# Kernel optimization log

Measured on AMD Instinct MI355X. Metric: run time of the kernel, lower is better.

The kernel has to match this reference:

```python
import jax, jax.numpy as jnp
from jax import lax
import numpy as np

# Constants from CVLNet utils (get_meter_per_pixel() and SatMap_original_sidelength)
METER_PER_PIXEL = 0.2
SATMAP_ORIGINAL_SIDELENGTH = 512.0
SHIFT_RANGE = 32
EPS = 1e-12


def _l2_normalize_per_sample(x):
    # F.normalize(x.reshape(B, -1)) : L2-normalize each sample over all elements
    B = x.shape[0]
    norm = jnp.linalg.norm(x.reshape(B, -1), axis=1)
    norm = jnp.maximum(norm, EPS).reshape((B,) + (1,) * (x.ndim - 1))
    return x / norm


def setup_inputs() -> dict:
    key = jax.random.key(0)
    k1, k2 = jax.random.split(key)
    grd_feature = jax.random.normal(k1, (4, 32, 64, 64), dtype=jnp.float32)   # (N,C,Hk,Wk)
    sat_feature = jax.random.normal(k2, (32, 32, 64, 64), dtype=jnp.float32)  # (M,C,Hs,Ws)
    return {"grd_feature": grd_feature, "sat_feature": sat_feature, "uncertainty": 1}


def reference(grd_feature, sat_feature, uncertainty):
    N, C, H_k, W_k = grd_feature.shape
    grd = _l2_normalize_per_sample(grd_feature)

    s = SHIFT_RANGE
    sat = jnp.pad(sat_feature, ((0, 0), (0, 0), (s, s), (s, s)))
    M, _, H_i, W_i = sat.shape
    sat = _l2_normalize_per_sample(sat)  # zero-padding does not change the norm

    # F.conv2d(sat.repeat(1,N,1,1), grd, groups=N) == plain cross-correlation of
    # every sat map with every grd template: output [M, N, Ho, Wo]
    corr = lax.conv_general_dilated(
        sat, grd, window_strides=(1, 1), padding='VALID',
        dimension_numbers=('NCHW', 'OIHW', 'NCHW'))

    # avg_pool2d(sat^2, (Hk,Wk), stride=1, divisor_override=1) summed over C ==
    # sliding-window sum of per-pixel squared norms
    s2 = jnp.sum(sat * sat, axis=1, keepdims=True)  # [M,1,Hi,Wi]
    partical = lax.reduce_window(s2, 0.0, lax.add,
                                 window_dimensions=(1, 1, H_k, W_k),
                                 window_strides=(1, 1, 1, 1), padding='VALID')
    denom = jnp.maximum(jnp.sqrt(partical) * uncertainty, EPS)
    corr = corr / denom

    similarity_matrix = jnp.max(corr, axis=(2, 3))  # [M,N]

    Wo = corr.shape[-1]
    max_index = jnp.argmax(corr.reshape(M, N, -1), axis=-1)
    row = (max_index // Wo).astype(jnp.float32)
    col = (max_index % Wo).astype(jnp.float32)
    half = Wo / 2.0
    max_pos = jnp.stack([-(row - half), col - half], axis=-1)  # [M,N,2]
    shift_meters = max_pos * METER_PER_PIXEL * SATMAP_ORIGINAL_SIDELENGTH / W_i
    return (similarity_matrix, shift_meters)
```

## Files before the change

kernel.cpp:

```cpp
#include <hip/hip_runtime.h>
#include <math.h>

#define N_GRD 4
#define M_SAT 32
#define C_CH  32
#define HK    64
#define WK    64
#define HO    65
#define WO    65
#define SAMPLE_ELEMS (C_CH * HK * WK)

typedef _Float16 h8 __attribute__((ext_vector_type(8)));
typedef float    f4 __attribute__((ext_vector_type(4)));
typedef unsigned int u32;

#define OFF_INV    0
#define OFF_S      64
#define OFF_CANDV  135264
#define OFF_CANDI  135776
#define OFF_DOTS   136288
#define OFF_PART   136800
#define OFF_G2F    956000
#define OFF_SH     1824352
#define G2_HALFS   1736704

#define G2V_BLOCKS 848
#define SH_BLOCKS  2048
#define ZERO_BLOCKS 801
#define PREP_BLOCKS (G2V_BLOCKS + SH_BLOCKS + M_SAT + N_GRD + ZERO_BLOCKS)

__global__ __launch_bounds__(256) void prep_kernel(const float* __restrict__ grd,
                                                   const float* __restrict__ sat,
                                                   _Float16* __restrict__ g2,
                                                   _Float16* __restrict__ sh,
                                                   float* __restrict__ S,
                                                   float* __restrict__ inv,
                                                   float* __restrict__ partial,
                                                   float* __restrict__ dots) {
    const int bx = blockIdx.x;
    const int tid = threadIdx.x;
    __shared__ float s2[64][65];

    if (bx < G2V_BLOCKS) {
        int g = bx * 256 + tid;
        int t0 = g * 2;
        int js0 = t0 % 106;
        int r = t0 / 106;
        int n  = r & 3;
        int i  = (r >> 2) & 63;
        int cq = (r >> 8) & 7;
        int cp = r >> 11;
        int j0 = js0 - 16 - cp;
        const float* gb = grd + (((size_t)n * 32 + cq * 4) * 64 + i) * 64;
        h8 hv;
#pragma unroll
        for (int c = 0; c < 4; ++c) {
            float v0 = (j0 >= 0 && j0 < 64) ? gb[c * 4096 + j0] : 0.0f;
            float v1 = (j0 + 1 >= 0 && j0 + 1 < 64) ? gb[c * 4096 + j0 + 1] : 0.0f;
            hv[c]     = (_Float16)v0;
            hv[c + 4] = (_Float16)v1;
        }
        *(h8*)(g2 + (size_t)g * 8) = hv;
        return;
    }
    if (bx < G2V_BLOCKS + SH_BLOCKS) {
        int idx = (bx - G2V_BLOCKS) * 256 + tid;
        int gr = idx & 31;
        int r  = (idx >> 5) & 63;
        int cq = (idx >> 11) & 7;
        int mm = idx >> 14;
        const float* sp = sat + (((size_t)mm * 32 + cq * 4) * 64 + r) * 64 + gr * 2;
        float2 v0 = *(const float2*)(sp);
        float2 v1 = *(const float2*)(sp + 4096);
        float2 v2 = *(const float2*)(sp + 8192);
        float2 v3 = *(const float2*)(sp + 12288);
        h8 hv = {(_Float16)v0.x, (_Float16)v1.x, (_Float16)v2.x, (_Float16)v3.x,
                 (_Float16)v0.y, (_Float16)v1.y, (_Float16)v2.y, (_Float16)v3.y};
        *(h8*)(sh + (size_t)idx * 8) = hv;
        return;
    }
    if (bx < G2V_BLOCKS + SH_BLOCKS + M_SAT) {
        const int m = bx - G2V_BLOCKS - SH_BLOCKS;
        const float* base = sat + (size_t)m * SAMPLE_ELEMS;
#pragma unroll 1
        for (int g = 0; g < 4; ++g) {
            int p0 = (g * 256 + tid) * 4;
            float sx = 0.f, sy = 0.f, sz = 0.f, sw = 0.f;
            for (int c = 0; c < C_CH; ++c) {
                float4 v = *(const float4*)(base + c * 4096 + p0);
                sx += v.x * v.x; sy += v.y * v.y; sz += v.z * v.z; sw += v.w * v.w;
            }
            int rr = p0 >> 6, cc = p0 & 63;
            s2[rr][cc] = sx; s2[rr][cc + 1] = sy; s2[rr][cc + 2] = sz; s2[rr][cc + 3] = sw;
        }
        __syncthreads();
        if (tid < 64) {
            int r = tid; float run = 0.0f;
            for (int w = 0; w < 64; ++w) { run += s2[r][w]; s2[r][w] = run; }
        }
        __syncthreads();
        if (tid < 64) {
            int c = tid; float run = 0.0f;
            for (int h = 0; h < 64; ++h) { run += s2[h][c]; s2[h][c] = run; }
        }
        __syncthreads();
        if (tid == 0)
            inv[N_GRD + m] = 1.0f / fmaxf(sqrtf(s2[63][63]), 1e-12f);
        float* Sm = S + (size_t)m * (HO * WO);
        for (int p = tid; p < HO * WO; p += 256) {
            int r = p / 65, c = p - r * 65;
            Sm[p] = (r == 0 || c == 0) ? 0.0f : s2[r - 1][c - 1];
        }
        return;
    }
    if (bx < G2V_BLOCKS + SH_BLOCKS + M_SAT + N_GRD) {
        const int b = bx - G2V_BLOCKS - SH_BLOCKS - M_SAT;
        const float4* v = reinterpret_cast<const float4*>(grd + (size_t)b * SAMPLE_ELEMS);
        float ss = 0.0f;
        for (int p = tid; p < SAMPLE_ELEMS / 4; p += 256) {
            float4 q = v[p];
            ss += q.x * q.x + q.y * q.y + q.z * q.z + q.w * q.w;
        }
        for (int off = 32; off > 0; off >>= 1) ss += __shfl_down(ss, off);
        __shared__ float ls[4];
        int lane = tid & 63, w = tid >> 6;
        if (lane == 0) ls[w] = ss;
        __syncthreads();
        if (tid == 0)
            inv[b] = 1.0f / fmaxf(sqrtf(ls[0] + ls[1] + ls[2] + ls[3]), 1e-12f);
        return;
    }
    {
        int idx = (bx - G2V_BLOCKS - SH_BLOCKS - M_SAT - N_GRD) * 256 + tid;
        f4 z = {0.f, 0.f, 0.f, 0.f};
        if (idx < 204800)            *(f4*)(partial + (size_t)idx * 4) = z;
        else if (idx - 204800 < 128) *(f4*)(dots + (size_t)(idx - 204800) * 4) = z;
    }
}

__global__ __launch_bounds__(256, 2) void corr_mfma_kernel(const _Float16* __restrict__ sh,
                                                           const _Float16* __restrict__ g2,
                                                           float* __restrict__ partial) {
    __shared__ __align__(16) char lds[79104];
    char* AB = lds;
    char* BB = lds + 48384;

    const int m  = blockIdx.x;
    const int xs = blockIdx.y;
    const int z  = blockIdx.z;
    const int h  = z & 1;
    const int qt = z >> 1;

    const int x00 = (xs < 4) ? 16 * xs : 49;
    const int qb  = (xs < 4) ? 16 * xs : 48;
    const int xoff = x00 - qb;
    const int qstage = qb + 40 * h;

    const int tid  = threadIdx.x;
    const int w    = tid >> 6;
    const int lane = tid & 63;
    const int s    = lane & 15;
    const int u    = lane >> 4;
    const int cp   = (s + xoff) & 1;

    f4 acc[5][4];
#pragma unroll
    for (int t = 0; t < 5; ++t)
#pragma unroll
        for (int n = 0; n < 4; ++n) { acc[t][n][0]=0.f; acc[t][n][1]=0.f; acc[t][n][2]=0.f; acc[t][n][3]=0.f; }

    const int woff = (16 - xoff + cp + 2 * u - s) * 8;
    const char* Blane = BB + w * 3840 + cp * 1920 + woff;
    const int abase0 = s * 336 + u * 16;
    const int q2base = qstage >> 1;

    size_t bsrc[4];
    bool bs_on[4];
#pragma unroll
    for (int k = 0; k < 4; ++k) {
        int idx = k * 64 + lane;
        bs_on[k] = idx < 240;
        int cpp = idx / 120; int rm = idx - cpp * 120;
        int nn = rm / 30;    int gg = rm - nn * 30;
        bsrc[k] = (size_t)cpp * 868352 + (size_t)nn * 424
                + (size_t)(gg + 20 * h) * 8 + (size_t)w * 27136;
    }

    auto stageA = [&](int cq) {
        for (int k = 0; k < 11; ++k) {
            int idx = k * 256 + tid;
            if (idx < 2688) {
                u32 r = (u32)idx / 21u;
                u32 g = (u32)idx - r * 21u;
                int q2 = q2base + (int)g;
                bool valid = (g < 20u) & (r >= 32u) & (r < 96u) & (q2 >= 16) & (q2 < 48);
                const _Float16* src = valid
                    ? sh + ((((size_t)m * 8 + cq) * 64 + (r - 32)) * 32 + (q2 - 16)) * 8
                    : g2;
                __builtin_amdgcn_global_load_lds(
                    (const __attribute__((address_space(1))) u32*)(const void*)src,
                    (__attribute__((address_space(3))) u32*)(void*)(AB + k * 4096 + w * 1024),
                    16, 0, 0);
            }
        }
    };

    auto stageB = [&](int cq, int ii, int bsel) {
        asm volatile("s_waitcnt lgkmcnt(0)" ::: "memory");
        char* dst0 = BB + bsel * 15360 + w * 3840;
        const size_t add = (size_t)cq * 108544 + (size_t)ii * 1696;
#pragma unroll
        for (int k = 0; k < 4; ++k) {
            if (bs_on[k])
                __builtin_amdgcn_global_load_lds(
                    (const __attribute__((address_space(1))) u32*)(const void*)(g2 + bsrc[k] + add),
                    (__attribute__((address_space(3))) u32*)(void*)(dst0 + k * 1024),
                    16, 0, 0);
        }
    };

    auto compute = [&](int ii, int bsel) {
        const char* Ab = AB + abase0 + (w * 16 + ii) * 336;
        const char* Bb = Blane + bsel * 15360;
#pragma unroll
        for (int qs = 0; qs < 5; ++qs) {
            h8 a[5]; h8 bfr[4];
#pragma unroll
            for (int n = 0; n < 4; ++n) bfr[n] = *(const h8*)(Bb + qs * 64 + n * 480);
#pragma unroll
            for (int t = 0; t < 5; ++t) a[t] = *(const h8*)(Ab + qs * 64 + t * 5376);
#pragma unroll
            for (int t = 0; t < 5; ++t)
#pragma unroll
                for (int n = 0; n < 4; ++n)
                    acc[t][n] = __builtin_amdgcn_mfma_f32_16x16x32_f16(a[t], bfr[n], acc[t][n], 0, 0, 0);
        }
    };

    for (int cqi = 0; cqi < 2; ++cqi) {
        const int cq = qt * 2 + cqi;
        __syncthreads();
        stageA(cq);
        stageB(cq, 0, 0);
        __syncthreads();
#pragma unroll 1
        for (int iip = 0; iip < 8; ++iip) {
            const int ii0 = 2 * iip;
            stageB(cq, ii0 + 1, 1);
            asm volatile("s_waitcnt vmcnt(4)" ::: "memory");
            compute(ii0, 0);
            if (iip < 7) {
                stageB(cq, ii0 + 2, 0);
                asm volatile("s_waitcnt vmcnt(4)" ::: "memory");
            } else {
                asm volatile("s_waitcnt vmcnt(0)" ::: "memory");
            }
            compute(ii0 + 1, 1);
        }
    }

    float* red = (float*)lds;
#pragma unroll
    for (int t = 0; t < 5; ++t) {
        __syncthreads();
#pragma unroll
        for (int nn = 0; nn < 4; ++nn)
            *(f4*)(red + ((nn * 4 + w) * 64 + lane) * 4) = acc[t][nn];
        __syncthreads();
        {
            int nn = tid >> 6, ln = tid & 63;
            f4 sum = *(f4*)(red + ((nn * 4 + 0) * 64 + ln) * 4);
            sum = sum + *(f4*)(red + ((nn * 4 + 1) * 64 + ln) * 4);
            sum = sum + *(f4*)(red + ((nn * 4 + 2) * 64 + ln) * 4);
            sum = sum + *(f4*)(red + ((nn * 4 + 3) * 64 + ln) * 4);
            int ss = ln & 15, uu = ln >> 4;
            float* dst = partial + ((size_t)(m * 4 + nn)) * 6400
                         + (xs * 16 + ss) * 80 + t * 16 + uu * 4;
#pragma unroll
            for (int l = 0; l < 4; ++l) atomicAdd(dst + l, sum[l]);
        }
    }
}

__global__ __launch_bounds__(256) void epilogue_kernel(const float* __restrict__ partial,
                                                       const float* __restrict__ S,
                                                       const float* __restrict__ inv,
                                                       const int* __restrict__ unc,
                                                       float* __restrict__ candv,
                                                       int* __restrict__ candi) {
    const int b = blockIdx.x;
    const int m = b >> 2, n = b & 3;
    const int tid = threadIdx.x;
    const float uu = (float)unc[0];
    const float sc = inv[n] * inv[N_GRD + m];
    const float isn = inv[N_GRD + m];
    const float* Sm = S + (size_t)m * 4225;
    const float* pb = partial + (size_t)(m * 4 + n) * 6400;

    float best = -3.4e38f;
    int bidx = 0x7fffffff;
    for (int pp = tid; pp < 4225; pp += 256) {
        int x = pp / 65, y = pp - x * 65;
        int xsl = (x == 64) ? 79 : x;
        float raw = pb[xsl * 80 + y];
        float num = raw * sc;
        int r0 = max(0, y - 32), r1 = min(64, y + 32);
        int q0 = max(0, x - 32), q1 = min(64, x + 32);
        float ps = Sm[r1 * 65 + q1] - Sm[r0 * 65 + q1] - Sm[r1 * 65 + q0] + Sm[r0 * 65 + q0];
        float denom = fmaxf(sqrtf(ps) * isn * uu, 1e-12f);
        float v = num / denom;
        int p = y * 65 + x;
        if (v > best || (v == best && p < bidx)) { best = v; bidx = p; }
    }
    __shared__ float bv[256]; __shared__ int bi[256];
    __shared__ float cv[256]; __shared__ int ci[256];
    __shared__ int winner;
    bv[tid] = best; bi[tid] = bidx;
    __syncthreads();
    for (int round = 0; round < 4; ++round) {
        cv[tid] = bv[tid]; ci[tid] = bi[tid];
        __syncthreads();
        for (int st = 128; st > 0; st >>= 1) {
            if (tid < st) {
                float ov = cv[tid + st]; int oi = ci[tid + st];
                if (ov > cv[tid] || (ov == cv[tid] && oi < ci[tid])) { cv[tid] = ov; ci[tid] = oi; }
            }
            __syncthreads();
        }
        if (tid == 0) { candv[b * 4 + round] = cv[0]; candi[b * 4 + round] = ci[0]; winner = ci[0]; }
        __syncthreads();
        if (bi[tid] == winner) bv[tid] = -3.4e38f;
        __syncthreads();
    }
}

__global__ __launch_bounds__(256) void refine_dot_kernel(const float* __restrict__ grd,
                                                         const float* __restrict__ sat,
                                                         const float* __restrict__ candv,
                                                         const int* __restrict__ candi,
                                                         float* __restrict__ dots) {
    const int b = blockIdx.x;
    const int k = blockIdx.y;
    const int cq = blockIdx.z;
    const int m = b >> 2, n = b & 3;
    float v0 = candv[b * 4];
    float thr = v0 - (0.02f * fabsf(v0) + 1e-4f);
    if (k > 0 && candv[b * 4 + k] < thr) return;
    int p = candi[b * 4 + k];
    int y = p / 65, x = p - y * 65;
    const int tid = threadIdx.x, lane = tid & 63, w = tid >> 6;
    const int ilo = max(0, 32 - y), ihi = min(64, 96 - y);
    int xj = x + lane - 32;
    float acc = 0.0f;
    if (xj >= 0 && xj < 64) {
        const float* sm = sat + (size_t)m * SAMPLE_ELEMS;
        const float* gn = grd + (size_t)n * SAMPLE_ELEMS;
        for (int cc = 0; cc < 4; ++cc) {
            const int cbase = (cq * 4 + cc) << 12;
            const float* sp = sm + cbase + xj + ((y - 32) << 6);
            const float* gp = gn + cbase + lane;
            for (int i = ilo + w; i < ihi; i += 4)
                acc = fmaf(sp[i << 6], gp[i << 6], acc);
        }
    }
    for (int off = 32; off > 0; off >>= 1) acc += __shfl_down(acc, off);
    __shared__ float ls[4];
    if (lane == 0) ls[w] = acc;
    __syncthreads();
    if (tid == 0) atomicAdd(&dots[b * 4 + k], ls[0] + ls[1] + ls[2] + ls[3]);
}

__global__ __launch_bounds__(128) void refine_pick_kernel(const float* __restrict__ S,
                                                          const float* __restrict__ inv,
                                                          const int* __restrict__ unc,
                                                          const float* __restrict__ candv,
                                                          const int* __restrict__ candi,
                                                          const float* __restrict__ dots,
                                                          float* __restrict__ out) {
    int b = threadIdx.x;
    if (b >= 128) return;
    const int m = b >> 2, n = b & 3;
    const float uu = (float)unc[0];
    const float sc = inv[n] * inv[N_GRD + m];
    const float isn = inv[N_GRD + m];
    const float* Sm = S + (size_t)m * 4225;
    float v0 = candv[b * 4];
    float thr = v0 - (0.02f * fabsf(v0) + 1e-4f);
    float bestv = -3.4e38f; int bestp = 0x7fffffff;
    for (int k = 0; k < 4; ++k) {
        if (k > 0 && candv[b * 4 + k] < thr) break;
        int p = candi[b * 4 + k];
        int y = p / 65, x = p - y * 65;
        int r0 = max(0, y - 32), r1 = min(64, y + 32);
        int q0 = max(0, x - 32), q1 = min(64, x + 32);
        float ps = Sm[r1 * 65 + q1] - Sm[r0 * 65 + q1] - Sm[r1 * 65 + q0] + Sm[r0 * 65 + q0];
        float denom = fmaxf(sqrtf(ps) * isn * uu, 1e-12f);
        float v = dots[b * 4 + k] * sc / denom;
        if (v > bestv || (v == bestv && p < bestp)) { bestv = v; bestp = p; }
    }
    out[b] = bestv;
    int row = bestp / 65, col = bestp - row * 65;
    float pr = -((float)row - 32.5f);
    float pc = (float)col - 32.5f;
    out[128 + b * 2 + 0] = ((pr * 0.2f) * 512.0f) * (1.0f / 128.0f);
    out[128 + b * 2 + 1] = ((pc * 0.2f) * 512.0f) * (1.0f / 128.0f);
}

extern "C" void kernel_launch(void* const* d_in, const int* in_sizes, int n_in,
                              void* d_out, int out_size, void* d_ws, size_t ws_size,
                              hipStream_t stream) {
    const float* grd = (const float*)d_in[0];
    const float* sat = (const float*)d_in[1];
    const int*   unc = (const int*)d_in[2];
    float* out = (float*)d_out;
    float* ws  = (float*)d_ws;

    float* inv     = ws + OFF_INV;
    float* S       = ws + OFF_S;
    float* candv   = ws + OFF_CANDV;
    int*   candi   = (int*)(ws + OFF_CANDI);
    float* dots    = ws + OFF_DOTS;
    float* partial = ws + OFF_PART;
    _Float16* g2   = (_Float16*)(ws + OFF_G2F);
    _Float16* sh   = (_Float16*)(ws + OFF_SH);

    prep_kernel<<<PREP_BLOCKS, 256, 0, stream>>>(grd, sat, g2, sh, S, inv, partial, dots);
    corr_mfma_kernel<<<dim3(M_SAT, 5, 8), 256, 0, stream>>>(sh, g2, partial);
    epilogue_kernel<<<M_SAT * N_GRD, 256, 0, stream>>>(partial, S, inv, unc, candv, candi);
    refine_dot_kernel<<<dim3(128, 4, 8), 256, 0, stream>>>(grd, sat, candv, candi, dots);
    refine_pick_kernel<<<1, 128, 0, stream>>>(S, inv, unc, candv, candi, dots, out);
}
```

Baseline: 336.8 us.

## Parallelize squared-norm prefix, move integral image to epilogue, fuse pick via last-block

The per-pixel channel squared-sum now runs across 256 blocks instead of 32 single blocks that did the serial prefix scans, and writes a raw map to global memory. The 2D prefix sum is computed in the epilogue kernel in LDS, once per (m,n) block, which removes the long-tail prep blocks. The refine_pick kernel is folded into refine_dot with a last-block-done atomic counter, saving one launch. The cost is redundant prefix scans in the epilogue (4x per sat map), plus an extra global atomic and fences per refine block.

```diff
diff --git a/kernel.cpp b/kernel.cpp
--- a/kernel.cpp
+++ b/kernel.cpp
@@ -22,24 +22,26 @@
 #define OFF_PART   136800
 #define OFF_G2F    956000
 #define OFF_SH     1824352
+#define OFF_S2G    3921504
 #define G2_HALFS   1736704
 
 #define G2V_BLOCKS 848
 #define SH_BLOCKS  2048
+#define S2P_BLOCKS 256
 #define ZERO_BLOCKS 801
-#define PREP_BLOCKS (G2V_BLOCKS + SH_BLOCKS + M_SAT + N_GRD + ZERO_BLOCKS)
+#define PREP_BLOCKS (G2V_BLOCKS + SH_BLOCKS + S2P_BLOCKS + N_GRD + ZERO_BLOCKS)
 
 __global__ __launch_bounds__(256) void prep_kernel(const float* __restrict__ grd,
                                                    const float* __restrict__ sat,
                                                    _Float16* __restrict__ g2,
                                                    _Float16* __restrict__ sh,
-                                                   float* __restrict__ S,
+                                                   float* __restrict__ s2g,
                                                    float* __restrict__ inv,
                                                    float* __restrict__ partial,
-                                                   float* __restrict__ dots) {
+                                                   float* __restrict__ dots,
+                                                   float* __restrict__ cntf) {
     const int bx = blockIdx.x;
     const int tid = threadIdx.x;
-    __shared__ float s2[64][65];
 
     if (bx < G2V_BLOCKS) {
         int g = bx * 256 + tid;
@@ -79,42 +81,23 @@
         *(h8*)(sh + (size_t)idx * 8) = hv;
         return;
     }
-    if (bx < G2V_BLOCKS + SH_BLOCKS + M_SAT) {
-        const int m = bx - G2V_BLOCKS - SH_BLOCKS;
-        const float* base = sat + (size_t)m * SAMPLE_ELEMS;
-#pragma unroll 1
-        for (int g = 0; g < 4; ++g) {
-            int p0 = (g * 256 + tid) * 4;
-            float sx = 0.f, sy = 0.f, sz = 0.f, sw = 0.f;
-            for (int c = 0; c < C_CH; ++c) {
-                float4 v = *(const float4*)(base + c * 4096 + p0);
-                sx += v.x * v.x; sy += v.y * v.y; sz += v.z * v.z; sw += v.w * v.w;
-            }
-            int rr = p0 >> 6, cc = p0 & 63;
-            s2[rr][cc] = sx; s2[rr][cc + 1] = sy; s2[rr][cc + 2] = sz; s2[rr][cc + 3] = sw;
-        }
-        __syncthreads();
-        if (tid < 64) {
-            int r = tid; float run = 0.0f;
-            for (int w = 0; w < 64; ++w) { run += s2[r][w]; s2[r][w] = run; }
-        }
-        __syncthreads();
-        if (tid < 64) {
-            int c = tid; float run = 0.0f;
-            for (int h = 0; h < 64; ++h) { run += s2[h][c]; s2[h][c] = run; }
-        }
-        __syncthreads();
-        if (tid == 0)
-            inv[N_GRD + m] = 1.0f / fmaxf(sqrtf(s2[63][63]), 1e-12f);
-        float* Sm = S + (size_t)m * (HO * WO);
-        for (int p = tid; p < HO * WO; p += 256) {
-            int r = p / 65, c = p - r * 65;
-            Sm[p] = (r == 0 || c == 0) ? 0.0f : s2[r - 1][c - 1];
-        }
+    if (bx < G2V_BLOCKS + SH_BLOCKS + S2P_BLOCKS) {
+        int blk = bx - G2V_BLOCKS - SH_BLOCKS;
+        int m = blk >> 3, sl = blk & 7;
+        int px0 = sl * 512 + tid * 2;
+        const float* base = sat + (size_t)m * SAMPLE_ELEMS + px0;
+        float sA = 0.0f, sB = 0.0f;
+        for (int c = 0; c < C_CH; ++c) {
+            float2 v = *(const float2*)(base + c * 4096);
+            sA += v.x * v.x;
+            sB += v.y * v.y;
+        }
+        s2g[(size_t)m * 4096 + px0]     = sA;
+        s2g[(size_t)m * 4096 + px0 + 1] = sB;
         return;
     }
-    if (bx < G2V_BLOCKS + SH_BLOCKS + M_SAT + N_GRD) {
-        const int b = bx - G2V_BLOCKS - SH_BLOCKS - M_SAT;
+    if (bx < G2V_BLOCKS + SH_BLOCKS + S2P_BLOCKS + N_GRD) {
+        const int b = bx - G2V_BLOCKS - SH_BLOCKS - S2P_BLOCKS;
         const float4* v = reinterpret_cast<const float4*>(grd + (size_t)b * SAMPLE_ELEMS);
         float ss = 0.0f;
         for (int p = tid; p < SAMPLE_ELEMS / 4; p += 256) {
@@ -131,10 +114,11 @@
         return;
     }
     {
-        int idx = (bx - G2V_BLOCKS - SH_BLOCKS - M_SAT - N_GRD) * 256 + tid;
+        int idx = (bx - G2V_BLOCKS - SH_BLOCKS - S2P_BLOCKS - N_GRD) * 256 + tid;
         f4 z = {0.f, 0.f, 0.f, 0.f};
-        if (idx < 204800)            *(f4*)(partial + (size_t)idx * 4) = z;
-        else if (idx - 204800 < 128) *(f4*)(dots + (size_t)(idx - 204800) * 4) = z;
+        if (idx < 204800)                 *(f4*)(partial + (size_t)idx * 4) = z;
+        else if (idx - 204800 < 128)      *(f4*)(dots + (size_t)(idx - 204800) * 4) = z;
+        else if (idx - 204800 == 128)     *(f4*)cntf = z;
     }
 }
 
@@ -283,18 +267,42 @@
 }
 
 __global__ __launch_bounds__(256) void epilogue_kernel(const float* __restrict__ partial,
-                                                       const float* __restrict__ S,
-                                                       const float* __restrict__ inv,
+                                                       const float* __restrict__ s2g,
+                                                       float* __restrict__ S,
+                                                       float* __restrict__ inv,
                                                        const int* __restrict__ unc,
                                                        float* __restrict__ candv,
                                                        int* __restrict__ candi) {
     const int b = blockIdx.x;
     const int m = b >> 2, n = b & 3;
     const int tid = threadIdx.x;
+    __shared__ float P[64][65];
+
+    const float* sg = s2g + (size_t)m * 4096;
+    for (int idx = tid; idx < 4096; idx += 256) P[idx >> 6][idx & 63] = sg[idx];
+    __syncthreads();
+    if (tid < 64) {
+        int r = tid; float run = 0.0f;
+        for (int w = 0; w < 64; ++w) { run += P[r][w]; P[r][w] = run; }
+    }
+    __syncthreads();
+    if (tid < 64) {
+        int c = tid; float run = 0.0f;
+        for (int h = 0; h < 64; ++h) { run += P[h][c]; P[h][c] = run; }
+    }
+    __syncthreads();
+    const float isn = 1.0f / fmaxf(sqrtf(P[63][63]), 1e-12f);
+    if (n == 0) {
+        if (tid == 0) inv[N_GRD + m] = isn;
+        float* Sm = S + (size_t)m * (HO * WO);
+        for (int p = tid; p < HO * WO; p += 256) {
+            int r = p / 65, c = p - r * 65;
+            Sm[p] = (r == 0 || c == 0) ? 0.0f : P[r - 1][c - 1];
+        }
+    }
+
     const float uu = (float)unc[0];
-    const float sc = inv[n] * inv[N_GRD + m];
-    const float isn = inv[N_GRD + m];
-    const float* Sm = S + (size_t)m * 4225;
+    const float sc = inv[n] * isn;
     const float* pb = partial + (size_t)(m * 4 + n) * 6400;
 
     float best = -3.4e38f;
@@ -306,7 +314,11 @@
         float num = raw * sc;
         int r0 = max(0, y - 32), r1 = min(64, y + 32);
         int q0 = max(0, x - 32), q1 = min(64, x + 32);
-        float ps = Sm[r1 * 65 + q1] - Sm[r0 * 65 + q1] - Sm[r1 * 65 + q0] + Sm[r0 * 65 + q0];
+        float s11 = P[r1 - 1][q1 - 1];
+        float s01 = (r0 == 0) ? 0.0f : P[r0 - 1][q1 - 1];
+        float s10 = (q0 == 0) ? 0.0f : P[r1 - 1][q0 - 1];
+        float s00 = (r0 == 0 || q0 == 0) ? 0.0f : P[r0 - 1][q0 - 1];
+        float ps = s11 - s01 - s10 + s00;
         float denom = fmaxf(sqrtf(ps) * isn * uu, 1e-12f);
         float v = num / denom;
         int p = y * 65 + x;
@@ -338,72 +350,85 @@
                                                          const float* __restrict__ sat,
                                                          const float* __restrict__ candv,
                                                          const int* __restrict__ candi,
-                                                         float* __restrict__ dots) {
+                                                         float* __restrict__ dots,
+                                                         const float* __restrict__ S,
+                                                         const float* __restrict__ inv,
+                                                         const int* __restrict__ unc,
+                                                         unsigned* __restrict__ cnt,
+                                                         float* __restrict__ out) {
     const int b = blockIdx.x;
     const int k = blockIdx.y;
     const int cq = blockIdx.z;
     const int m = b >> 2, n = b & 3;
+    const int tid = threadIdx.x, lane = tid & 63, w = tid >> 6;
+    __shared__ float ls[4];
+    __shared__ int lastf;
+
     float v0 = candv[b * 4];
     float thr = v0 - (0.02f * fabsf(v0) + 1e-4f);
-    if (k > 0 && candv[b * 4 + k] < thr) return;
-    int p = candi[b * 4 + k];
-    int y = p / 65, x = p - y * 65;
-    const int tid = threadIdx.x, lane = tid & 63, w = tid >> 6;
-    const int ilo = max(0, 32 - y), ihi = min(64, 96 - y);
-    int xj = x + lane - 32;
-    float acc = 0.0f;
-    if (xj >= 0 && xj < 64) {
-        const float* sm = sat + (size_t)m * SAMPLE_ELEMS;
-        const float* gn = grd + (size_t)n * SAMPLE_ELEMS;
-        for (int cc = 0; cc < 4; ++cc) {
-            const int cbase = (cq * 4 + cc) << 12;
-            const float* sp = sm + cbase + xj + ((y - 32) << 6);
-            const float* gp = gn + cbase + lane;
-            for (int i = ilo + w; i < ihi; i += 4)
-                acc = fmaf(sp[i << 6], gp[i << 6], acc);
-        }
-    }
-    for (int off = 32; off > 0; off >>= 1) acc += __shfl_down(acc, off);
-    __shared__ float ls[4];
-    if (lane == 0) ls[w] = acc;
-    __syncthreads();
-    if (tid == 0) atomicAdd(&dots[b * 4 + k], ls[0] + ls[1] + ls[2] + ls[3]);
-}
-
-__global__ __launch_bounds__(128) void refine_pick_kernel(const float* __restrict__ S,
-                                                          const float* __restrict__ inv,
-                                                          const int* __restrict__ unc,
-                                                          const float* __restrict__ candv,
-                                                          const int* __restrict__ candi,
-                                                          const float* __restrict__ dots,
-                                                          float* __restrict__ out) {
-    int b = threadIdx.x;
-    if (b >= 128) return;
-    const int m = b >> 2, n = b & 3;
-    const float uu = (float)unc[0];
-    const float sc = inv[n] * inv[N_GRD + m];
-    const float isn = inv[N_GRD + m];
-    const float* Sm = S + (size_t)m * 4225;
-    float v0 = candv[b * 4];
-    float thr = v0 - (0.02f * fabsf(v0) + 1e-4f);
-    float bestv = -3.4e38f; int bestp = 0x7fffffff;
-    for (int k = 0; k < 4; ++k) {
-        if (k > 0 && candv[b * 4 + k] < thr) break;
+    bool skip = (k > 0 && candv[b * 4 + k] < thr);
+    if (!skip) {
         int p = candi[b * 4 + k];
         int y = p / 65, x = p - y * 65;
-        int r0 = max(0, y - 32), r1 = min(64, y + 32);
-        int q0 = max(0, x - 32), q1 = min(64, x + 32);
-        float ps = Sm[r1 * 65 + q1] - Sm[r0 * 65 + q1] - Sm[r1 * 65 + q0] + Sm[r0 * 65 + q0];
-        float denom = fmaxf(sqrtf(ps) * isn * uu, 1e-12f);
-        float v = dots[b * 4 + k] * sc / denom;
-        if (v > bestv || (v == bestv && p < bestp)) { bestv = v; bestp = p; }
-    }
-    out[b] = bestv;
-    int row = bestp / 65, col = bestp - row * 65;
-    float pr = -((float)row - 32.5f);
-    float pc = (float)col - 32.5f;
-    out[128 + b * 2 + 0] = ((pr * 0.2f) * 512.0f) * (1.0f / 128.0f);
-    out[128 + b * 2 + 1] = ((pc * 0.2f) * 512.0f) * (1.0f / 128.0f);
+        const int ilo = max(0, 32 - y), ihi = min(64, 96 - y);
+        int xj = x + lane - 32;
+        float acc = 0.0f;
+        if (xj >= 0 && xj < 64) {
+            const float* sm = sat + (size_t)m * SAMPLE_ELEMS;
+            const float* gn = grd + (size_t)n * SAMPLE_ELEMS;
+            for (int cc = 0; cc < 4; ++cc) {
+                const int cbase = (cq * 4 + cc) << 12;
+                const float* sp = sm + cbase + xj + ((y - 32) << 6);
+                const float* gp = gn + cbase + lane;
+                for (int i = ilo + w; i < ihi; i += 4)
+                    acc = fmaf(sp[i << 6], gp[i << 6], acc);
+            }
+        }
+        for (int off = 32; off > 0; off >>= 1) acc += __shfl_down(acc, off);
+        if (lane == 0) ls[w] = acc;
+        __syncthreads();
+        if (tid == 0) atomicAdd(&dots[b * 4 + k], ls[0] + ls[1] + ls[2] + ls[3]);
+    }
+
+    __syncthreads();
+    if (tid == 0) {
+        __threadfence();
+        unsigned prev = atomicAdd(cnt, 1u);
+        lastf = (prev == 128u * 4u * 8u - 1u) ? 1 : 0;
+    }
+    __syncthreads();
+    if (!lastf) return;
+    __threadfence();
+    if (tid >= 128) return;
+    {
+        const int bb = tid;
+        const int mm = bb >> 2, nn = bb & 3;
+        const volatile float* dv = dots;
+        const float uu = (float)unc[0];
+        const float scp = inv[nn] * inv[N_GRD + mm];
+        const float isn = inv[N_GRD + mm];
+        const float* Sm = S + (size_t)mm * 4225;
+        float w0 = candv[bb * 4];
+        float thr2 = w0 - (0.02f * fabsf(w0) + 1e-4f);
+        float bestv = -3.4e38f; int bestp = 0x7fffffff;
+        for (int kk = 0; kk < 4; ++kk) {
+            if (kk > 0 && candv[bb * 4 + kk] < thr2) break;
+            int p = candi[bb * 4 + kk];
+            int y = p / 65, x = p - y * 65;
+            int r0 = max(0, y - 32), r1 = min(64, y + 32);
+            int q0 = max(0, x - 32), q1 = min(64, x + 32);
+            float ps = Sm[r1 * 65 + q1] - Sm[r0 * 65 + q1] - Sm[r1 * 65 + q0] + Sm[r0 * 65 + q0];
+            float denom = fmaxf(sqrtf(ps) * isn * uu, 1e-12f);
+            float v = dv[bb * 4 + kk] * scp / denom;
+            if (v > bestv || (v == bestv && p < bestp)) { bestv = v; bestp = p; }
+        }
+        out[bb] = bestv;
+        int row = bestp / 65, col = bestp - row * 65;
+        float pr = -((float)row - 32.5f);
+        float pc = (float)col - 32.5f;
+        out[128 + bb * 2 + 0] = ((pr * 0.2f) * 512.0f) * (1.0f / 128.0f);
+        out[128 + bb * 2 + 1] = ((pc * 0.2f) * 512.0f) * (1.0f / 128.0f);
+    }
 }
 
 extern "C" void kernel_launch(void* const* d_in, const int* in_sizes, int n_in,
@@ -416,6 +441,7 @@
     float* ws  = (float*)d_ws;
 
     float* inv     = ws + OFF_INV;
+    float* cntf    = ws + 48;
     float* S       = ws + OFF_S;
     float* candv   = ws + OFF_CANDV;
     int*   candi   = (int*)(ws + OFF_CANDI);
@@ -423,10 +449,11 @@
     float* partial = ws + OFF_PART;
     _Float16* g2   = (_Float16*)(ws + OFF_G2F);
     _Float16* sh   = (_Float16*)(ws + OFF_SH);
-
-    prep_kernel<<<PREP_BLOCKS, 256, 0, stream>>>(grd, sat, g2, sh, S, inv, partial, dots);
+    float* s2g     = ws + OFF_S2G;
+
+    prep_kernel<<<PREP_BLOCKS, 256, 0, stream>>>(grd, sat, g2, sh, s2g, inv, partial, dots, cntf);
     corr_mfma_kernel<<<dim3(M_SAT, 5, 8), 256, 0, stream>>>(sh, g2, partial);
-    epilogue_kernel<<<M_SAT * N_GRD, 256, 0, stream>>>(partial, S, inv, unc, candv, candi);
-    refine_dot_kernel<<<dim3(128, 4, 8), 256, 0, stream>>>(grd, sat, candv, candi, dots);
-    refine_pick_kernel<<<1, 128, 0, stream>>>(S, inv, unc, candv, candi, dots, out);
+    epilogue_kernel<<<M_SAT * N_GRD, 256, 0, stream>>>(partial, s2g, S, inv, unc, candv, candi);
+    refine_dot_kernel<<<dim3(128, 4, 8), 256, 0, stream>>>(grd, sat, candv, candi, dots,
+                                                           S, inv, unc, (unsigned*)cntf, out);
 }
```

Result: slower. 428.7 us (+27.3%).

## Replace atomic accumulation with per-split slabs reduced in epilogue; raise MFMA priority

Applied to the files above, without the earlier changes.

When the workspace is large enough, each of the 8 z-splits of the correlation kernel writes its partial tile with plain vector stores into its own slab, instead of four scalar atomicAdds per element into a shared buffer. The epilogue then sums the 8 slabs while it reads the result. The MFMA inner block is also wrapped in s_setprio to raise wave priority during compute. The trade is more workspace memory and more epilogue reads in exchange for removing atomic contention. The prep kernel still zeroes the old partial buffer, which is now unnecessary work.

```diff
diff --git a/kernel.cpp b/kernel.cpp
--- a/kernel.cpp
+++ b/kernel.cpp
@@ -22,6 +22,8 @@
 #define OFF_PART   136800
 #define OFF_G2F    956000
 #define OFF_SH     1824352
+#define OFF_SLAB   4052576
+#define ZSTRIDE    819200
 #define G2_HALFS   1736704
 
 #define G2V_BLOCKS 848
@@ -133,14 +135,15 @@
     {
         int idx = (bx - G2V_BLOCKS - SH_BLOCKS - M_SAT - N_GRD) * 256 + tid;
         f4 z = {0.f, 0.f, 0.f, 0.f};
-        if (idx < 204800)            *(f4*)(partial + (size_t)idx * 4) = z;
-        else if (idx - 204800 < 128) *(f4*)(dots + (size_t)(idx - 204800) * 4) = z;
+        if (idx < 204800)                 *(f4*)(partial + (size_t)idx * 4) = z;
+        else if (idx - 204800 < 128)      *(f4*)(dots + (size_t)(idx - 204800) * 4) = z;
     }
 }
 
 __global__ __launch_bounds__(256, 2) void corr_mfma_kernel(const _Float16* __restrict__ sh,
                                                            const _Float16* __restrict__ g2,
-                                                           float* __restrict__ partial) {
+                                                           float* __restrict__ partial,
+                                                           int zstride) {
     __shared__ __align__(16) char lds[79104];
     char* AB = lds;
     char* BB = lds + 48384;
@@ -229,11 +232,13 @@
             for (int n = 0; n < 4; ++n) bfr[n] = *(const h8*)(Bb + qs * 64 + n * 480);
 #pragma unroll
             for (int t = 0; t < 5; ++t) a[t] = *(const h8*)(Ab + qs * 64 + t * 5376);
+            __builtin_amdgcn_s_setprio(1);
 #pragma unroll
             for (int t = 0; t < 5; ++t)
 #pragma unroll
                 for (int n = 0; n < 4; ++n)
                     acc[t][n] = __builtin_amdgcn_mfma_f32_16x16x32_f16(a[t], bfr[n], acc[t][n], 0, 0, 0);
+            __builtin_amdgcn_s_setprio(0);
         }
     };
 
@@ -274,10 +279,15 @@
             sum = sum + *(f4*)(red + ((nn * 4 + 2) * 64 + ln) * 4);
             sum = sum + *(f4*)(red + ((nn * 4 + 3) * 64 + ln) * 4);
             int ss = ln & 15, uu = ln >> 4;
-            float* dst = partial + ((size_t)(m * 4 + nn)) * 6400
+            float* dst = partial + (size_t)z * (size_t)zstride
+                         + ((size_t)(m * 4 + nn)) * 6400
                          + (xs * 16 + ss) * 80 + t * 16 + uu * 4;
-#pragma unroll
-            for (int l = 0; l < 4; ++l) atomicAdd(dst + l, sum[l]);
+            if (zstride != 0) {
+                *(f4*)dst = sum;
+            } else {
+#pragma unroll
+                for (int l = 0; l < 4; ++l) atomicAdd(dst + l, sum[l]);
+            }
         }
     }
 }
@@ -287,7 +297,8 @@
                                                        const float* __restrict__ inv,
                                                        const int* __restrict__ unc,
                                                        float* __restrict__ candv,
-                                                       int* __restrict__ candi) {
+                                                       int* __restrict__ candi,
+                                                       int zstride) {
     const int b = blockIdx.x;
     const int m = b >> 2, n = b & 3;
     const int tid = threadIdx.x;
@@ -302,7 +313,13 @@
     for (int pp = tid; pp < 4225; pp += 256) {
         int x = pp / 65, y = pp - x * 65;
         int xsl = (x == 64) ? 79 : x;
-        float raw = pb[xsl * 80 + y];
+        int off = xsl * 80 + y;
+        float raw = pb[off];
+        if (zstride != 0) {
+#pragma unroll
+            for (int zz = 1; zz < 8; ++zz)
+                raw += pb[(size_t)zz * (size_t)zstride + off];
+        }
         float num = raw * sc;
         int r0 = max(0, y - 32), r1 = min(64, y + 32);
         int q0 = max(0, x - 32), q1 = min(64, x + 32);
@@ -424,9 +441,13 @@
     _Float16* g2   = (_Float16*)(ws + OFF_G2F);
     _Float16* sh   = (_Float16*)(ws + OFF_SH);
 
+    const size_t need = ((size_t)OFF_SLAB + 8ull * ZSTRIDE) * sizeof(float);
+    const int zstride = (ws_size >= need) ? ZSTRIDE : 0;
+    float* corrout = zstride ? (ws + OFF_SLAB) : partial;
+
     prep_kernel<<<PREP_BLOCKS, 256, 0, stream>>>(grd, sat, g2, sh, S, inv, partial, dots);
-    corr_mfma_kernel<<<dim3(M_SAT, 5, 8), 256, 0, stream>>>(sh, g2, partial);
-    epilogue_kernel<<<M_SAT * N_GRD, 256, 0, stream>>>(partial, S, inv, unc, candv, candi);
+    corr_mfma_kernel<<<dim3(M_SAT, 5, 8), 256, 0, stream>>>(sh, g2, corrout, zstride);
+    epilogue_kernel<<<M_SAT * N_GRD, 256, 0, stream>>>(corrout, S, inv, unc, candv, candi, zstride);
     refine_dot_kernel<<<dim3(128, 4, 8), 256, 0, stream>>>(grd, sat, candv, candi, dots);
     refine_pick_kernel<<<1, 128, 0, stream>>>(S, inv, unc, candv, candi, dots, out);
 }
```

Result: faster. 316.8 us (-5.9%).
